# Kernel optimization log

Measured on AMD Instinct MI355X. Metric: run time of the kernel, lower is better.

The kernel has to match this reference:

```python
import jax, jax.numpy as jnp
import numpy as np

D = 1024
F = 256
EPS = 1e-5


def layer_norm(x, g, b):
    mu = jnp.mean(x, axis=-1, keepdims=True)
    var = jnp.mean((x - mu) ** 2, axis=-1, keepdims=True)
    return (x - mu) * jax.lax.rsqrt(var + EPS) * g + b


def setup_inputs() -> dict:
    key = jax.random.key(0)
    ks = jax.random.split(key, 8)
    B, S = 4, 4096
    return {
        "bottom_up_input": jax.random.normal(ks[0], (B, S, D), dtype=jnp.float32),
        "top_down_prediction": jax.random.normal(ks[1], (B, S, D), dtype=jnp.float32),
        "W_spec": jax.random.normal(ks[2], (2 * F, D), dtype=jnp.float32) * 0.02,
        "log_decay": jnp.linspace(-3.0, -0.001, F, dtype=jnp.float32),
        "frequencies": jax.random.normal(ks[3], (F,), dtype=jnp.float32) * 0.1,
        "W_from": jax.random.normal(ks[4], (D, 2 * F), dtype=jnp.float32) * 0.02,
        "ln1_g": jnp.ones((D,), jnp.float32),
        "ln1_b": jnp.zeros((D,), jnp.float32),
        "W1": jax.random.normal(ks[5], (D, D), dtype=jnp.float32) * 0.02,
        "b1": jnp.zeros((D,), jnp.float32),
        "W2": jax.random.normal(ks[6], (D, D), dtype=jnp.float32) * 0.02,
        "b2": jnp.zeros((D,), jnp.float32),
        "ln2_g": jnp.ones((D,), jnp.float32),
        "ln2_b": jnp.zeros((D,), jnp.float32),
        "error_weight": jnp.asarray(0.1, jnp.float32),
    }


def spectral_conv(x, W_spec, log_decay, frequencies, W_from, ln1_g, ln1_b):
    # x: [B,S,D]
    x = layer_norm(x, ln1_g, ln1_b)
    B, S, _ = x.shape
    spectral = jnp.einsum('bsd,fd->bsf', x, W_spec)  # [B,S,2F]
    u = jax.lax.complex(spectral[..., :F], spectral[..., F:])  # [B,S,F] complex
    decay = jax.nn.sigmoid(log_decay)
    omega = jnp.tanh(frequencies) * 0.1  # dt = 1.0
    rot = jax.lax.complex(jnp.cos(omega), jnp.sin(omega))  # [F]
    A = (decay * rot).astype(jnp.complex64)  # [F]
    # kernel[t] = A^t * rot, built with cumprod as in the original
    ones = jnp.ones((1, F), dtype=A.dtype)
    A_seq = jnp.broadcast_to(A[None, :], (S - 1, F))
    powers = jnp.cumprod(jnp.concatenate([ones, A_seq], axis=0), axis=0)  # [S,F]
    kernel = (powers * rot[None, :])[None]  # [1,S,F]
    n_fft = 2 * S
    U_f = jnp.fft.fft(u, n=n_fft, axis=1)
    K_f = jnp.fft.fft(kernel, n=n_fft, axis=1)
    y = jnp.fft.ifft(U_f * K_f, n=n_fft, axis=1)[:, :S, :]  # [B,S,F]
    spectral_out = jnp.concatenate([y.real, y.imag], axis=-1)  # [B,S,2F]
    return jnp.einsum('bsf,df->bsd', spectral_out, W_from)


def reference(bottom_up_input, top_down_prediction, W_spec, log_decay, frequencies,
              W_from, ln1_g, ln1_b, W1, b1, W2, b2, ln2_g, ln2_b, error_weight):
    bu_repr = spectral_conv(bottom_up_input, W_spec, log_decay, frequencies,
                            W_from, ln1_g, ln1_b)
    error = jnp.clip(bu_repr - top_down_prediction, -1.0, 1.0)
    corrected = bu_repr - jax.nn.sigmoid(error_weight) * error
    prediction_error = jnp.clip(jnp.mean(error ** 2), 0.0, 1.0)
    h = jax.nn.gelu(jnp.einsum('bsd,ed->bse', corrected, W1) + b1, approximate=False)
    h = jnp.einsum('bsd,ed->bse', h, W2) + b2
    next_prediction = layer_norm(h, ln2_g, ln2_b)
    return corrected, next_prediction, prediction_error
```

## Files before the change

kernel.cpp:

```cpp
#include <hip/hip_runtime.h>
#include <math.h>

#define Dn 1024
#define Fn 256
#define Sn 4096
#define Bn 4
#define Mn (Bn*Sn)
#define CHn 8
#define NCn (Sn/CHn)

typedef __bf16 bf16x8 __attribute__((ext_vector_type(8)));
typedef float  f32x4  __attribute__((ext_vector_type(4)));

__device__ inline unsigned short f2bf(float f) {
  unsigned int u = __float_as_uint(f);
  u += 0x7fffu + ((u >> 16) & 1u);
  return (unsigned short)(u >> 16);
}
__device__ inline float bf2f(unsigned short s) {
  return __uint_as_float(((unsigned int)s) << 16);
}

__device__ inline void async16(const void* g, void* l) {
  __builtin_amdgcn_global_load_lds(
      (__attribute__((address_space(1))) void*)(g),
      (__attribute__((address_space(3))) void*)(l), 16, 0, 0);
}

#define WAITVM(n) __builtin_amdgcn_s_waitcnt(0xF70 | (n))
#define BARRIER() asm volatile("s_barrier" ::: "memory")

__global__ __launch_bounds__(256) void ln1_conv(
    const float* __restrict__ x, const float* __restrict__ g,
    const float* __restrict__ b, unsigned short* __restrict__ out,
    const float* __restrict__ wspec, const float* __restrict__ wfrom,
    const float* __restrict__ w1, const float* __restrict__ w2,
    unsigned short* __restrict__ o_spec, unsigned short* __restrict__ o_from,
    unsigned short* __restrict__ o_w1, unsigned short* __restrict__ o_w2) {
  int tid = threadIdx.x;
  int gid = blockIdx.x * 256 + tid;
  o_w1[gid] = f2bf(w1[gid]);
  o_w2[gid] = f2bf(w2[gid]);
  if (gid < 524288) {
    o_spec[gid] = f2bf(wspec[gid]);
    o_from[gid] = f2bf(wfrom[gid]);
  }

  int wid = tid >> 6, lane = tid & 63;
  int row = blockIdx.x * 4 + wid;
  const float4* xr = (const float4*)x + (size_t)row * 256;
  float4 v[4];
  float s = 0.0f, ss = 0.0f;
  #pragma unroll
  for (int k = 0; k < 4; k++) {
    v[k] = xr[lane + 64 * k];
    s  += v[k].x + v[k].y + v[k].z + v[k].w;
    ss += v[k].x * v[k].x + v[k].y * v[k].y + v[k].z * v[k].z + v[k].w * v[k].w;
  }
  #pragma unroll
  for (int o = 32; o; o >>= 1) {
    s  += __shfl_xor(s, o);
    ss += __shfl_xor(ss, o);
  }
  float mu  = s * (1.0f / Dn);
  float var = ss * (1.0f / Dn) - mu * mu;
  float rs  = rsqrtf(var + 1e-5f);
  ushort4* orow = (ushort4*)out + (size_t)row * 256;
  #pragma unroll
  for (int k = 0; k < 4; k++) {
    float4 gv = ((const float4*)g)[lane + 64 * k];
    float4 bv = ((const float4*)b)[lane + 64 * k];
    ushort4 w;
    w.x = f2bf((v[k].x - mu) * rs * gv.x + bv.x);
    w.y = f2bf((v[k].y - mu) * rs * gv.y + bv.y);
    w.z = f2bf((v[k].z - mu) * rs * gv.z + bv.z);
    w.w = f2bf((v[k].w - mu) * rs * gv.w + bv.w);
    orow[lane + 64 * k] = w;
  }
}

__global__ __launch_bounds__(256) void ln2_err(
    const unsigned short* __restrict__ h, const float* __restrict__ g,
    const float* __restrict__ b, float* __restrict__ out,
    const float* __restrict__ errAcc, float* __restrict__ outErr) {
  int tid = threadIdx.x;
  if (blockIdx.x == 0 && tid == 0) {
    float m = errAcc[0] * (1.0f / 16777216.0f);
    outErr[0] = fminf(fmaxf(m, 0.0f), 1.0f);
  }
  int wid = tid >> 6, lane = tid & 63;
  int row = blockIdx.x * 4 + wid;
  const ushort4* xr = (const ushort4*)h + (size_t)row * 256;
  float4 v[4];
  float s = 0.0f, ss = 0.0f;
  #pragma unroll
  for (int k = 0; k < 4; k++) {
    ushort4 u = xr[lane + 64 * k];
    v[k].x = bf2f(u.x); v[k].y = bf2f(u.y); v[k].z = bf2f(u.z); v[k].w = bf2f(u.w);
    s  += v[k].x + v[k].y + v[k].z + v[k].w;
    ss += v[k].x * v[k].x + v[k].y * v[k].y + v[k].z * v[k].z + v[k].w * v[k].w;
  }
  #pragma unroll
  for (int o = 32; o; o >>= 1) {
    s  += __shfl_xor(s, o);
    ss += __shfl_xor(ss, o);
  }
  float mu  = s * (1.0f / Dn);
  float var = ss * (1.0f / Dn) - mu * mu;
  float rs  = rsqrtf(var + 1e-5f);
  float4* orow = (float4*)out + (size_t)row * 256;
  #pragma unroll
  for (int k = 0; k < 4; k++) {
    float4 gv = ((const float4*)g)[lane + 64 * k];
    float4 bv = ((const float4*)b)[lane + 64 * k];
    float4 w;
    w.x = (v[k].x - mu) * rs * gv.x + bv.x;
    w.y = (v[k].y - mu) * rs * gv.y + bv.y;
    w.z = (v[k].z - mu) * rs * gv.z + bv.z;
    w.w = (v[k].w - mu) * rs * gv.w + bv.w;
    orow[lane + 64 * k] = w;
  }
}

template <int MODE>
__global__ __launch_bounds__(256, 4) void gemm_bt(
    const unsigned short* __restrict__ A, const unsigned short* __restrict__ Bw,
    int K, int N,
    float* __restrict__ outF, unsigned short* __restrict__ outH,
    const float* __restrict__ td, const float* __restrict__ bias,
    const float* __restrict__ ew, float* __restrict__ errAcc) {
  __shared__ unsigned short As[2 * 4096];
  __shared__ unsigned short Bs[2 * 4096];
  __shared__ float red[4];

  int tid = threadIdx.x;
  int wid = tid >> 6, lane = tid & 63;
  int wm = wid >> 1, wn = wid & 1;
  int quad = lane >> 4, l16 = lane & 15;

  int g = blockIdx.x + gridDim.x * blockIdx.y;
  int nbn = gridDim.x;
  int gh = g >> 3;
  int bn = gh % nbn;
  int bm = (g & 7) + (gh / nbn) * 8;

  int r_lo = lane >> 2;
  int c8   = (lane & 3) * 8;

  const unsigned short* Abase = A + (size_t)bm * 128 * K;
  const unsigned short* Bbase = Bw + (size_t)bn * 128 * K;

  f32x4 acc[4][4] = {};

  const int T = K >> 5;
  auto issue = [&](int t, int stg) {
    int k0 = t << 5;
    #pragma unroll
    for (int s = 0; s < 2; ++s) {
      int chunk = s * 4 + wid;
      int r = chunk * 16 + r_lo;
      async16(Abase + (size_t)r * K + k0 + c8, As + stg * 4096 + chunk * 512);
      async16(Bbase + (size_t)r * K + k0 + c8, Bs + stg * 4096 + chunk * 512);
    }
  };

  issue(0, 0);

  for (int k = 0; k < T; ++k) {
    WAITVM(0);
    BARRIER();
    if (k + 1 < T) issue(k + 1, (k + 1) & 1);

    const unsigned short* Ab = As + (k & 1) * 4096;
    const unsigned short* Bb = Bs + (k & 1) * 4096;
    bf16x8 af[4], bf[4];
    #pragma unroll
    for (int i = 0; i < 4; i++)
      af[i] = *(const bf16x8*)(Ab + (wm * 64 + i * 16 + l16) * 32 + quad * 8);
    #pragma unroll
    for (int j = 0; j < 4; j++)
      bf[j] = *(const bf16x8*)(Bb + (wn * 64 + j * 16 + l16) * 32 + quad * 8);
    #pragma unroll
    for (int i = 0; i < 4; i++)
      #pragma unroll
      for (int j = 0; j < 4; j++)
        acc[i][j] = __builtin_amdgcn_mfma_f32_16x16x32_bf16(af[i], bf[j], acc[i][j], 0, 0, 0);
  }

  float esum = 0.0f;
  float sigw = 0.0f;
  if (MODE == 1) sigw = 1.0f / (1.0f + expf(-ew[0]));

  #pragma unroll
  for (int i = 0; i < 4; i++) {
    int row_base = bm * 128 + wm * 64 + i * 16 + quad * 4;
    #pragma unroll
    for (int j = 0; j < 4; j++) {
      int col = bn * 128 + wn * 64 + j * 16 + l16;
      #pragma unroll
      for (int r = 0; r < 4; r++) {
        size_t idx = (size_t)(row_base + r) * N + col;
        float v = acc[i][j][r];
        if (MODE == 0) {
          outH[idx] = f2bf(v);
        } else if (MODE == 1) {
          float e = v - td[idx];
          e = fminf(fmaxf(e, -1.0f), 1.0f);
          float corr = v - sigw * e;
          outF[idx] = corr;
          outH[idx] = f2bf(corr);
          esum += e * e;
        } else if (MODE == 2) {
          float h = v + bias[col];
          float gel = 0.5f * h * (1.0f + erff(h * 0.70710678118654752f));
          outH[idx] = f2bf(gel);
        } else if (MODE == 3) {
          outF[idx] = v + bias[col];
        } else {
          outH[idx] = f2bf(v + bias[col]);
        }
      }
    }
  }

  if (MODE == 1) {
    #pragma unroll
    for (int o = 32; o; o >>= 1) esum += __shfl_down(esum, o);
    if (lane == 0) red[wid] = esum;
    __syncthreads();
    if (tid == 0) atomicAdd(errAcc, red[0] + red[1] + red[2] + red[3]);
  }
}

__global__ __launch_bounds__(256) void scan_partial(
    const unsigned short* __restrict__ spec, const float* __restrict__ log_decay,
    const float* __restrict__ freq, float2* __restrict__ chunkfin) {
  int tid = threadIdx.x, wid = tid >> 6, lane = tid & 63;
  int chunk = blockIdx.x * 4 + wid;
  int b = chunk >> 9, c = chunk & (NCn - 1);
  int f0 = lane * 4;
  float Are[4], Aim[4];
  #pragma unroll
  for (int k = 0; k < 4; k++) {
    float dec = 1.0f / (1.0f + expf(-log_decay[f0 + k]));
    float om  = tanhf(freq[f0 + k]) * 0.1f;
    Are[k] = dec * cosf(om); Aim[k] = dec * sinf(om);
  }
  const unsigned short* u = spec + ((size_t)b * Sn + (size_t)c * CHn) * 512;
  float sre[4] = {0, 0, 0, 0}, sim[4] = {0, 0, 0, 0};
  #pragma unroll
  for (int t = 0; t < CHn; t++) {
    ushort4 ur = *(const ushort4*)(u + (size_t)t * 512 + f0);
    ushort4 ui = *(const ushort4*)(u + (size_t)t * 512 + 256 + f0);
    float urf[4] = {bf2f(ur.x), bf2f(ur.y), bf2f(ur.z), bf2f(ur.w)};
    float uif[4] = {bf2f(ui.x), bf2f(ui.y), bf2f(ui.z), bf2f(ui.w)};
    #pragma unroll
    for (int k = 0; k < 4; k++) {
      float nre = Are[k] * sre[k] - Aim[k] * sim[k] + urf[k];
      float nim = Are[k] * sim[k] + Aim[k] * sre[k] + uif[k];
      sre[k] = nre; sim[k] = nim;
    }
  }
  #pragma unroll
  for (int k = 0; k < 4; k++)
    chunkfin[((size_t)(b * 256 + f0 + k)) * NCn + c] = make_float2(sre[k], sim[k]);
}

__global__ __launch_bounds__(512) void scan_carry(
    const float* __restrict__ log_decay, const float* __restrict__ freq,
    const float2* __restrict__ chunkfin, float2* __restrict__ carries) {
  __shared__ float2 buf[NCn];
  int bf = blockIdx.x;
  int f = bf & 255;
  int c = threadIdx.x;
  float dec = 1.0f / (1.0f + expf(-log_decay[f]));
  float om  = tanhf(freq[f]) * 0.1f;
  float Mre = dec * cosf(om), Mim = dec * sinf(om);
  #pragma unroll
  for (int i = 0; i < 3; i++) {
    float nr = Mre * Mre - Mim * Mim;
    float ni = 2.0f * Mre * Mim;
    Mre = nr; Mim = ni;
  }
  float2 v = chunkfin[(size_t)bf * NCn + c];
  buf[c] = v;
  __syncthreads();
  for (int s = 1; s < NCn; s <<= 1) {
    float2 w = (c >= s) ? buf[c - s] : make_float2(0.0f, 0.0f);
    __syncthreads();
    v.x += Mre * w.x - Mim * w.y;
    v.y += Mre * w.y + Mim * w.x;
    buf[c] = v;
    __syncthreads();
    float nr = Mre * Mre - Mim * Mim;
    float ni = 2.0f * Mre * Mim;
    Mre = nr; Mim = ni;
  }
  float2 e = (c == 0) ? make_float2(0.0f, 0.0f) : buf[c - 1];
  carries[(size_t)bf * NCn + c] = e;
}

__global__ __launch_bounds__(256) void scan_final(
    const unsigned short* __restrict__ spec, const float* __restrict__ log_decay,
    const float* __restrict__ freq, const float2* __restrict__ carries,
    unsigned short* __restrict__ outH) {
  int tid = threadIdx.x, wid = tid >> 6, lane = tid & 63;
  int chunk = blockIdx.x * 4 + wid;
  int b = chunk >> 9, c = chunk & (NCn - 1);
  int f0 = lane * 4;
  float Are[4], Aim[4], Rre[4], Rim[4], sre[4], sim[4];
  #pragma unroll
  for (int k = 0; k < 4; k++) {
    float dec = 1.0f / (1.0f + expf(-log_decay[f0 + k]));
    float om  = tanhf(freq[f0 + k]) * 0.1f;
    Rre[k] = cosf(om); Rim[k] = sinf(om);
    Are[k] = dec * Rre[k]; Aim[k] = dec * Rim[k];
    float2 s0 = carries[((size_t)(b * 256 + f0 + k)) * NCn + c];
    sre[k] = s0.x; sim[k] = s0.y;
  }
  const unsigned short* u = spec + ((size_t)b * Sn + (size_t)c * CHn) * 512;
  unsigned short* o = outH + ((size_t)b * Sn + (size_t)c * CHn) * 512;
  #pragma unroll
  for (int t = 0; t < CHn; t++) {
    ushort4 ur = *(const ushort4*)(u + (size_t)t * 512 + f0);
    ushort4 ui = *(const ushort4*)(u + (size_t)t * 512 + 256 + f0);
    float urf[4] = {bf2f(ur.x), bf2f(ur.y), bf2f(ur.z), bf2f(ur.w)};
    float uif[4] = {bf2f(ui.x), bf2f(ui.y), bf2f(ui.z), bf2f(ui.w)};
    ushort4 wr, wi;
    unsigned short* wrp = &wr.x;
    unsigned short* wip = &wi.x;
    #pragma unroll
    for (int k = 0; k < 4; k++) {
      float nre = Are[k] * sre[k] - Aim[k] * sim[k] + urf[k];
      float nim = Are[k] * sim[k] + Aim[k] * sre[k] + uif[k];
      sre[k] = nre; sim[k] = nim;
      wrp[k] = f2bf(Rre[k] * sre[k] - Rim[k] * sim[k]);
      wip[k] = f2bf(Rre[k] * sim[k] + Rim[k] * sre[k]);
    }
    *(ushort4*)(o + (size_t)t * 512 + f0) = wr;
    *(ushort4*)(o + (size_t)t * 512 + 256 + f0) = wi;
  }
}

extern "C" void kernel_launch(void* const* d_in, const int* in_sizes, int n_in,
                              void* d_out, int out_size, void* d_ws, size_t ws_size,
                              hipStream_t stream) {
  (void)in_sizes; (void)n_in; (void)out_size; (void)ws_size;
  const float* x     = (const float*)d_in[0];
  const float* td    = (const float*)d_in[1];
  const float* wspec = (const float*)d_in[2];
  const float* logd  = (const float*)d_in[3];
  const float* freq  = (const float*)d_in[4];
  const float* wfrom = (const float*)d_in[5];
  const float* g1    = (const float*)d_in[6];
  const float* b1ln  = (const float*)d_in[7];
  const float* W1    = (const float*)d_in[8];
  const float* b1    = (const float*)d_in[9];
  const float* W2    = (const float*)d_in[10];
  const float* b2    = (const float*)d_in[11];
  const float* g2    = (const float*)d_in[12];
  const float* b2ln  = (const float*)d_in[13];
  const float* ew    = (const float*)d_in[14];

  char* ws = (char*)d_ws;
  size_t off = 0;
  float* errAcc = (float*)(ws + off);              off += 256;
  unsigned short* wspec_h = (unsigned short*)(ws + off); off += (size_t)512 * 1024 * 2;
  unsigned short* wfrom_h = (unsigned short*)(ws + off); off += (size_t)1024 * 512 * 2;
  unsigned short* w1_h    = (unsigned short*)(ws + off); off += (size_t)1024 * 1024 * 2;
  unsigned short* w2_h    = (unsigned short*)(ws + off); off += (size_t)1024 * 1024 * 2;
  unsigned short* xn_h   = (unsigned short*)(ws + off);
  unsigned short* corr_h = (unsigned short*)(ws + off);
  unsigned short* h2_h   = (unsigned short*)(ws + off); off += (size_t)Mn * 1024 * 2;
  unsigned short* spec  = (unsigned short*)(ws + off);
  unsigned short* h1_h  = (unsigned short*)(ws + off);  off += (size_t)Mn * 1024 * 2;
  unsigned short* so_h = (unsigned short*)(ws + off);  off += (size_t)Mn * 512 * 2;
  float2* chunkfin = (float2*)(ws + off);              off += (size_t)Bn * 256 * NCn * 8;
  float2* carries  = (float2*)(ws + off);              off += (size_t)Bn * 256 * NCn * 8;

  float* outCorr = (float*)d_out;
  float* outNP   = outCorr + (size_t)Mn * 1024;
  float* outErr  = outNP + (size_t)Mn * 1024;

  hipMemsetAsync(errAcc, 0, 4, stream);
  ln1_conv<<<4096, 256, 0, stream>>>(x, g1, b1ln, xn_h,
                                     wspec, wfrom, W1, W2,
                                     wspec_h, wfrom_h, w1_h, w2_h);
  gemm_bt<0><<<dim3(512 / 128, Mn / 128), 256, 0, stream>>>(
      xn_h, wspec_h, 1024, 512, nullptr, spec, nullptr, nullptr, nullptr, nullptr);
  scan_partial<<<512, 256, 0, stream>>>(spec, logd, freq, chunkfin);
  scan_carry<<<1024, 512, 0, stream>>>(logd, freq, chunkfin, carries);
  scan_final<<<512, 256, 0, stream>>>(spec, logd, freq, carries, so_h);
  gemm_bt<1><<<dim3(1024 / 128, Mn / 128), 256, 0, stream>>>(
      so_h, wfrom_h, 512, 1024, outCorr, corr_h, td, nullptr, ew, errAcc);
  gemm_bt<2><<<dim3(1024 / 128, Mn / 128), 256, 0, stream>>>(
      corr_h, w1_h, 1024, 1024, nullptr, h1_h, nullptr, b1, nullptr, nullptr);
  gemm_bt<4><<<dim3(1024 / 128, Mn / 128), 256, 0, stream>>>(
      h1_h, w2_h, 1024, 1024, nullptr, h2_h, nullptr, b2, nullptr, nullptr);
  ln2_err<<<4096, 256, 0, stream>>>(h2_h, g2, b2ln, outNP, errAcc, outErr);
}
```

Baseline: 450.7 us.

## Fuse three scan kernels into one cooperative kernel with grid syncs

Merges scan_partial, scan_carry and scan_final into one cooperative kernel that uses grid-wide syncs between phases. Spec values are held in registers across phases, so the second read of spec is gone. The carry phase now does a serial 4-element pre-reduction per thread and a 128-wide Hillis-Steele scan instead of a 512-wide one. The errAcc memset is folded into ln1_conv. This removes two kernel launches and a memset, in exchange for grid-sync overhead and the requirement that all 512 blocks be co-resident.

```diff
diff --git a/kernel.cpp b/kernel.cpp
--- a/kernel.cpp
+++ b/kernel.cpp
@@ -1,5 +1,8 @@
 #include <hip/hip_runtime.h>
+#include <hip/hip_cooperative_groups.h>
 #include <math.h>
+
+namespace cg = cooperative_groups;
 
 #define Dn 1024
 #define Fn 256
@@ -36,9 +39,11 @@
     const float* __restrict__ wspec, const float* __restrict__ wfrom,
     const float* __restrict__ w1, const float* __restrict__ w2,
     unsigned short* __restrict__ o_spec, unsigned short* __restrict__ o_from,
-    unsigned short* __restrict__ o_w1, unsigned short* __restrict__ o_w2) {
+    unsigned short* __restrict__ o_w1, unsigned short* __restrict__ o_w2,
+    float* __restrict__ errAcc) {
   int tid = threadIdx.x;
   int gid = blockIdx.x * 256 + tid;
+  if (gid == 0) errAcc[0] = 0.0f;
   o_w1[gid] = f2bf(w1[gid]);
   o_w2[gid] = f2bf(w2[gid]);
   if (gid < 524288) {
@@ -232,113 +237,132 @@
   }
 }
 
-__global__ __launch_bounds__(256) void scan_partial(
+__global__ __launch_bounds__(256) void scan_fused(
     const unsigned short* __restrict__ spec, const float* __restrict__ log_decay,
-    const float* __restrict__ freq, float2* __restrict__ chunkfin) {
+    const float* __restrict__ freq, float2* __restrict__ chunkfin,
+    float2* __restrict__ carries, unsigned short* __restrict__ outH) {
+  cg::grid_group grid = cg::this_grid();
+  __shared__ float2 ks[2][128];
+
   int tid = threadIdx.x, wid = tid >> 6, lane = tid & 63;
   int chunk = blockIdx.x * 4 + wid;
   int b = chunk >> 9, c = chunk & (NCn - 1);
   int f0 = lane * 4;
-  float Are[4], Aim[4];
-  #pragma unroll
-  for (int k = 0; k < 4; k++) {
-    float dec = 1.0f / (1.0f + expf(-log_decay[f0 + k]));
-    float om  = tanhf(freq[f0 + k]) * 0.1f;
-    Are[k] = dec * cosf(om); Aim[k] = dec * sinf(om);
-  }
+
+  ushort4 ur[CHn], ui[CHn];
   const unsigned short* u = spec + ((size_t)b * Sn + (size_t)c * CHn) * 512;
-  float sre[4] = {0, 0, 0, 0}, sim[4] = {0, 0, 0, 0};
   #pragma unroll
   for (int t = 0; t < CHn; t++) {
-    ushort4 ur = *(const ushort4*)(u + (size_t)t * 512 + f0);
-    ushort4 ui = *(const ushort4*)(u + (size_t)t * 512 + 256 + f0);
-    float urf[4] = {bf2f(ur.x), bf2f(ur.y), bf2f(ur.z), bf2f(ur.w)};
-    float uif[4] = {bf2f(ui.x), bf2f(ui.y), bf2f(ui.z), bf2f(ui.w)};
-    #pragma unroll
-    for (int k = 0; k < 4; k++) {
-      float nre = Are[k] * sre[k] - Aim[k] * sim[k] + urf[k];
-      float nim = Are[k] * sim[k] + Aim[k] * sre[k] + uif[k];
-      sre[k] = nre; sim[k] = nim;
-    }
-  }
-  #pragma unroll
-  for (int k = 0; k < 4; k++)
-    chunkfin[((size_t)(b * 256 + f0 + k)) * NCn + c] = make_float2(sre[k], sim[k]);
-}
-
-__global__ __launch_bounds__(512) void scan_carry(
-    const float* __restrict__ log_decay, const float* __restrict__ freq,
-    const float2* __restrict__ chunkfin, float2* __restrict__ carries) {
-  __shared__ float2 buf[NCn];
-  int bf = blockIdx.x;
-  int f = bf & 255;
-  int c = threadIdx.x;
-  float dec = 1.0f / (1.0f + expf(-log_decay[f]));
-  float om  = tanhf(freq[f]) * 0.1f;
-  float Mre = dec * cosf(om), Mim = dec * sinf(om);
-  #pragma unroll
-  for (int i = 0; i < 3; i++) {
-    float nr = Mre * Mre - Mim * Mim;
-    float ni = 2.0f * Mre * Mim;
-    Mre = nr; Mim = ni;
-  }
-  float2 v = chunkfin[(size_t)bf * NCn + c];
-  buf[c] = v;
-  __syncthreads();
-  for (int s = 1; s < NCn; s <<= 1) {
-    float2 w = (c >= s) ? buf[c - s] : make_float2(0.0f, 0.0f);
-    __syncthreads();
-    v.x += Mre * w.x - Mim * w.y;
-    v.y += Mre * w.y + Mim * w.x;
-    buf[c] = v;
-    __syncthreads();
-    float nr = Mre * Mre - Mim * Mim;
-    float ni = 2.0f * Mre * Mim;
-    Mre = nr; Mim = ni;
-  }
-  float2 e = (c == 0) ? make_float2(0.0f, 0.0f) : buf[c - 1];
-  carries[(size_t)bf * NCn + c] = e;
-}
-
-__global__ __launch_bounds__(256) void scan_final(
-    const unsigned short* __restrict__ spec, const float* __restrict__ log_decay,
-    const float* __restrict__ freq, const float2* __restrict__ carries,
-    unsigned short* __restrict__ outH) {
-  int tid = threadIdx.x, wid = tid >> 6, lane = tid & 63;
-  int chunk = blockIdx.x * 4 + wid;
-  int b = chunk >> 9, c = chunk & (NCn - 1);
-  int f0 = lane * 4;
-  float Are[4], Aim[4], Rre[4], Rim[4], sre[4], sim[4];
+    ur[t] = *(const ushort4*)(u + (size_t)t * 512 + f0);
+    ui[t] = *(const ushort4*)(u + (size_t)t * 512 + 256 + f0);
+  }
+  float Are[4], Aim[4], Rre[4], Rim[4];
   #pragma unroll
   for (int k = 0; k < 4; k++) {
     float dec = 1.0f / (1.0f + expf(-log_decay[f0 + k]));
     float om  = tanhf(freq[f0 + k]) * 0.1f;
     Rre[k] = cosf(om); Rim[k] = sinf(om);
     Are[k] = dec * Rre[k]; Aim[k] = dec * Rim[k];
-    float2 s0 = carries[((size_t)(b * 256 + f0 + k)) * NCn + c];
-    sre[k] = s0.x; sim[k] = s0.y;
-  }
-  const unsigned short* u = spec + ((size_t)b * Sn + (size_t)c * CHn) * 512;
-  unsigned short* o = outH + ((size_t)b * Sn + (size_t)c * CHn) * 512;
-  #pragma unroll
-  for (int t = 0; t < CHn; t++) {
-    ushort4 ur = *(const ushort4*)(u + (size_t)t * 512 + f0);
-    ushort4 ui = *(const ushort4*)(u + (size_t)t * 512 + 256 + f0);
-    float urf[4] = {bf2f(ur.x), bf2f(ur.y), bf2f(ur.z), bf2f(ur.w)};
-    float uif[4] = {bf2f(ui.x), bf2f(ui.y), bf2f(ui.z), bf2f(ui.w)};
-    ushort4 wr, wi;
-    unsigned short* wrp = &wr.x;
-    unsigned short* wip = &wi.x;
+  }
+  {
+    float sre[4] = {0, 0, 0, 0}, sim[4] = {0, 0, 0, 0};
+    #pragma unroll
+    for (int t = 0; t < CHn; t++) {
+      const unsigned short* urp = &ur[t].x;
+      const unsigned short* uip = &ui[t].x;
+      #pragma unroll
+      for (int k = 0; k < 4; k++) {
+        float nre = Are[k] * sre[k] - Aim[k] * sim[k] + bf2f(urp[k]);
+        float nim = Are[k] * sim[k] + Aim[k] * sre[k] + bf2f(uip[k]);
+        sre[k] = nre; sim[k] = nim;
+      }
+    }
+    #pragma unroll
+    for (int k = 0; k < 4; k++)
+      chunkfin[((size_t)(b * 256 + f0 + k)) * NCn + c] = make_float2(sre[k], sim[k]);
+  }
+  __threadfence();
+  grid.sync();
+  __threadfence();
+
+  {
+    int half = tid >> 7;
+    int pair = blockIdx.x * 2 + half;
+    int h = tid & 127;
+    int fb = pair & 255, pb = pair >> 8;
+    float dec = 1.0f / (1.0f + expf(-log_decay[fb]));
+    float om  = tanhf(freq[fb]) * 0.1f;
+    float Pre = dec * cosf(om), Pim = dec * sinf(om);
+    #pragma unroll
+    for (int i = 0; i < 3; i++) {
+      float nr = Pre * Pre - Pim * Pim, ni = 2.0f * Pre * Pim;
+      Pre = nr; Pim = ni;
+    }
+    const float2* cfb = chunkfin + (size_t)(pb * 256 + fb) * NCn + h * 4;
+    float2 cf0 = cfb[0], cf1 = cfb[1], cf2 = cfb[2], cf3 = cfb[3];
+    float2 S = cf0;
+    { float nx = Pre*S.x - Pim*S.y + cf1.x, ny = Pre*S.y + Pim*S.x + cf1.y; S.x=nx; S.y=ny; }
+    { float nx = Pre*S.x - Pim*S.y + cf2.x, ny = Pre*S.y + Pim*S.x + cf2.y; S.x=nx; S.y=ny; }
+    { float nx = Pre*S.x - Pim*S.y + cf3.x, ny = Pre*S.y + Pim*S.x + cf3.y; S.x=nx; S.y=ny; }
+    float Mre = Pre, Mim = Pim;
+    #pragma unroll
+    for (int i = 0; i < 2; i++) {
+      float nr = Mre * Mre - Mim * Mim, ni = 2.0f * Mre * Mim;
+      Mre = nr; Mim = ni;
+    }
+    ks[half][h] = S;
+    __syncthreads();
+    float2 v = S;
+    for (int s = 1; s < 128; s <<= 1) {
+      float2 w = (h >= s) ? ks[half][h - s] : make_float2(0.0f, 0.0f);
+      __syncthreads();
+      v.x += Mre * w.x - Mim * w.y;
+      v.y += Mre * w.y + Mim * w.x;
+      ks[half][h] = v;
+      __syncthreads();
+      float nr = Mre * Mre - Mim * Mim, ni = 2.0f * Mre * Mim;
+      Mre = nr; Mim = ni;
+    }
+    float2 e = (h == 0) ? make_float2(0.0f, 0.0f) : ks[half][h - 1];
+    float2* cw = carries + (size_t)(pb * 256 + fb) * NCn + h * 4;
+    cw[0] = e;
+    { float nx = Pre*e.x - Pim*e.y + cf0.x, ny = Pre*e.y + Pim*e.x + cf0.y; e.x=nx; e.y=ny; }
+    cw[1] = e;
+    { float nx = Pre*e.x - Pim*e.y + cf1.x, ny = Pre*e.y + Pim*e.x + cf1.y; e.x=nx; e.y=ny; }
+    cw[2] = e;
+    { float nx = Pre*e.x - Pim*e.y + cf2.x, ny = Pre*e.y + Pim*e.x + cf2.y; e.x=nx; e.y=ny; }
+    cw[3] = e;
+  }
+  __threadfence();
+  grid.sync();
+  __threadfence();
+
+  {
+    float sre[4], sim[4];
     #pragma unroll
     for (int k = 0; k < 4; k++) {
-      float nre = Are[k] * sre[k] - Aim[k] * sim[k] + urf[k];
-      float nim = Are[k] * sim[k] + Aim[k] * sre[k] + uif[k];
-      sre[k] = nre; sim[k] = nim;
-      wrp[k] = f2bf(Rre[k] * sre[k] - Rim[k] * sim[k]);
-      wip[k] = f2bf(Rre[k] * sim[k] + Rim[k] * sre[k]);
-    }
-    *(ushort4*)(o + (size_t)t * 512 + f0) = wr;
-    *(ushort4*)(o + (size_t)t * 512 + 256 + f0) = wi;
+      float2 s0 = carries[((size_t)(b * 256 + f0 + k)) * NCn + c];
+      sre[k] = s0.x; sim[k] = s0.y;
+    }
+    unsigned short* o = outH + ((size_t)b * Sn + (size_t)c * CHn) * 512;
+    #pragma unroll
+    for (int t = 0; t < CHn; t++) {
+      const unsigned short* urp = &ur[t].x;
+      const unsigned short* uip = &ui[t].x;
+      ushort4 wr, wi;
+      unsigned short* wrp = &wr.x;
+      unsigned short* wip = &wi.x;
+      #pragma unroll
+      for (int k = 0; k < 4; k++) {
+        float nre = Are[k] * sre[k] - Aim[k] * sim[k] + bf2f(urp[k]);
+        float nim = Are[k] * sim[k] + Aim[k] * sre[k] + bf2f(uip[k]);
+        sre[k] = nre; sim[k] = nim;
+        wrp[k] = f2bf(Rre[k] * sre[k] - Rim[k] * sim[k]);
+        wip[k] = f2bf(Rre[k] * sim[k] + Rim[k] * sre[k]);
+      }
+      *(ushort4*)(o + (size_t)t * 512 + f0) = wr;
+      *(ushort4*)(o + (size_t)t * 512 + 256 + f0) = wi;
+    }
   }
 }
 
@@ -382,15 +406,18 @@
   float* outNP   = outCorr + (size_t)Mn * 1024;
   float* outErr  = outNP + (size_t)Mn * 1024;
 
-  hipMemsetAsync(errAcc, 0, 4, stream);
   ln1_conv<<<4096, 256, 0, stream>>>(x, g1, b1ln, xn_h,
                                      wspec, wfrom, W1, W2,
-                                     wspec_h, wfrom_h, w1_h, w2_h);
+                                     wspec_h, wfrom_h, w1_h, w2_h, errAcc);
   gemm_bt<0><<<dim3(512 / 128, Mn / 128), 256, 0, stream>>>(
       xn_h, wspec_h, 1024, 512, nullptr, spec, nullptr, nullptr, nullptr, nullptr);
-  scan_partial<<<512, 256, 0, stream>>>(spec, logd, freq, chunkfin);
-  scan_carry<<<1024, 512, 0, stream>>>(logd, freq, chunkfin, carries);
-  scan_final<<<512, 256, 0, stream>>>(spec, logd, freq, carries, so_h);
+  {
+    const unsigned short* specc = spec;
+    void* kargs[] = {(void*)&specc, (void*)&logd, (void*)&freq,
+                     (void*)&chunkfin, (void*)&carries, (void*)&so_h};
+    hipLaunchCooperativeKernel((void*)scan_fused, dim3(512), dim3(256),
+                               kargs, 0, stream);
+  }
   gemm_bt<1><<<dim3(1024 / 128, Mn / 128), 256, 0, stream>>>(
       so_h, wfrom_h, 512, 1024, outCorr, corr_h, td, nullptr, ew, errAcc);
   gemm_bt<2><<<dim3(1024 / 128, Mn / 128), 256, 0, stream>>>(
```

Result: slower. 764.4 us (+69.6%).
